# Performance work log

Hardware: AMD Instinct MI355X
Metric: run time of the kernel (lower is better)

Reference implementation:

```python
import jax, jax.numpy as jnp
import numpy as np

B, N, K = 4, 50000, 128   # batch, surface points, deformation nodes
GD = 128                  # SDF grid resolution (D=H=W)


def setup_inputs() -> dict:
    key = jax.random.key(0)
    ks = jax.random.split(key, 7)
    constants = jax.random.normal(ks[0], (B, K), dtype=jnp.float32)
    scales = 0.05 + 0.25 * jax.random.uniform(ks[1], (B, K), dtype=jnp.float32)
    # proper-ish rotations via QR of random matrices
    M = jax.random.normal(ks[2], (B, K, 3, 3), dtype=jnp.float32)
    rotations, _ = jnp.linalg.qr(M)
    centers = jax.random.uniform(ks[3], (B, K, 3), dtype=jnp.float32, minval=-0.5, maxval=0.5)
    surface_samples = jax.random.uniform(ks[4], (B, N, 6), dtype=jnp.float32, minval=-0.5, maxval=0.5)
    grid = jax.random.normal(ks[5], (B, GD, GD, GD), dtype=jnp.float32)
    # world2grid maps world [-0.5,0.5] -> grid index [0, GD-1]
    w2g = np.zeros((B, 4, 4), dtype=np.float32)
    w2g[:, 0, 0] = w2g[:, 1, 1] = w2g[:, 2, 2] = float(GD - 1)
    w2g[:, :3, 3] = float(GD - 1) / 2.0
    w2g[:, 3, 3] = 1.0
    world2grid = jnp.asarray(w2g)
    return {"constants": constants, "scales": scales, "rotations": rotations,
            "centers": centers, "surface_samples": surface_samples,
            "grid": grid, "world2grid": world2grid}


def _trilinear_border(vol, xyz):
    """torch grid_sample (5D, bilinear, align_corners=True, border) for one batch.
    vol: (D,H,W); xyz: (N,3) normalized coords in [-1,1], order (x,y,z)."""
    D, H, W = vol.shape
    x = jnp.clip((xyz[:, 0] + 1.0) * 0.5 * (W - 1), 0.0, W - 1)
    y = jnp.clip((xyz[:, 1] + 1.0) * 0.5 * (H - 1), 0.0, H - 1)
    z = jnp.clip((xyz[:, 2] + 1.0) * 0.5 * (D - 1), 0.0, D - 1)
    x0 = jnp.floor(x); y0 = jnp.floor(y); z0 = jnp.floor(z)
    fx = x - x0; fy = y - y0; fz = z - z0
    x0i = x0.astype(jnp.int32); x1i = jnp.minimum(x0i + 1, W - 1)
    y0i = y0.astype(jnp.int32); y1i = jnp.minimum(y0i + 1, H - 1)
    z0i = z0.astype(jnp.int32); z1i = jnp.minimum(z0i + 1, D - 1)
    c000 = vol[z0i, y0i, x0i]; c001 = vol[z0i, y0i, x1i]
    c010 = vol[z0i, y1i, x0i]; c011 = vol[z0i, y1i, x1i]
    c100 = vol[z1i, y0i, x0i]; c101 = vol[z1i, y0i, x1i]
    c110 = vol[z1i, y1i, x0i]; c111 = vol[z1i, y1i, x1i]
    c00 = c000 * (1 - fx) + c001 * fx
    c01 = c010 * (1 - fx) + c011 * fx
    c10 = c100 * (1 - fx) + c101 * fx
    c11 = c110 * (1 - fx) + c111 * fx
    c0 = c00 * (1 - fy) + c01 * fy
    c1 = c10 * (1 - fy) + c11 * fy
    return c0 * (1 - fz) + c1 * fz


def reference(constants, scales, rotations, centers, surface_samples, grid, world2grid):
    pts = surface_samples[..., :3]                       # (B,N,3)
    diff = pts[:, :, None, :] - centers[:, None, :, :]   # (B,N,K,3)  == p - t_source
    d2 = jnp.sum(diff * diff, axis=-1)                   # (B,N,K)
    # sample_rbf_weights with use_constants=True
    w = jnp.exp(-d2 / (2.0 * scales * scales)[:, None, :]) * (constants * constants)[:, None, :]
    w = w / jnp.sum(w, axis=-1, keepdims=True)           # normalize over nodes

    # target = roll batch by -1 (source_idx+1 mod B)
    R_t = jnp.roll(rotations, -1, axis=0)
    R_rel = jnp.einsum('bkij,bklj->bkil', R_t, rotations)       # R_target @ R_source^T
    c_t = jnp.roll(centers, -1, axis=0)
    transformed = jnp.einsum('bkij,bnkj->bnki', R_rel, diff) + c_t[:, None, :, :]
    blended = jnp.einsum('bnk,bnki->bni', w, transformed)        # (B,N,3)

    w2g_t = jnp.roll(world2grid, -1, axis=0)
    A = w2g_t[:, :3, :3]
    t = w2g_t[:, :3, 3]
    gcs = jnp.einsum('bij,bnj->bni', A, blended) + t[:, None, :]  # grid coords (x,y,z)

    D, H, W = grid.shape[1], grid.shape[2], grid.shape[3]
    denom = jnp.array([W - 1, H - 1, D - 1], dtype=gcs.dtype)
    gcs = 2.0 * (gcs / denom) - 1.0                               # normalize to [-1,1]

    grid_t = jnp.roll(grid, -1, axis=0)
    sdf = jax.vmap(_trilinear_border)(grid_t, gcs)                # (B,N)
    return jnp.sum(jnp.mean(sdf * sdf, axis=1))
```

## Files before the change

### kernel.cpp

```cpp
#include <hip/hip_runtime.h>
#include <stdint.h>

#define K_   128
#define GD_  128
#define PSTR 20
#define KPW  32

static __device__ __forceinline__ float fast_exp2(float x) {
#if __has_builtin(__builtin_amdgcn_exp2f)
    return __builtin_amdgcn_exp2f(x);
#else
    return exp2f(x);
#endif
}

__global__ void surf_param_kernel(
    const float* __restrict__ constants,
    const float* __restrict__ scales,
    const float* __restrict__ rotations,
    const float* __restrict__ centers,
    const float* __restrict__ w2g,
    float* __restrict__ params,
    float* __restrict__ out,
    int B)
{
    int idx = blockIdx.x * blockDim.x + threadIdx.x;
    if (idx == 0) out[0] = 0.0f;
    if (idx >= B * K_) return;
    int b = idx / K_, k = idx - b * K_;
    int bn = (b + 1 == B) ? 0 : (b + 1);
    const float L2E = 1.4426950408889634f;

    const float* R  = rotations + (size_t)(b  * K_ + k) * 9;
    const float* Rt = rotations + (size_t)(bn * K_ + k) * 9;
    float m[9];
#pragma unroll
    for (int i = 0; i < 3; ++i)
#pragma unroll
        for (int l = 0; l < 3; ++l)
            m[i * 3 + l] = Rt[i * 3 + 0] * R[l * 3 + 0]
                         + Rt[i * 3 + 1] * R[l * 3 + 1]
                         + Rt[i * 3 + 2] * R[l * 3 + 2];

    const float* Aw = w2g + (size_t)bn * 16;
    float G[9], A[9] = {Aw[0], Aw[1], Aw[2], Aw[4], Aw[5], Aw[6], Aw[8], Aw[9], Aw[10]};
    float T[3] = {Aw[3], Aw[7], Aw[11]};
#pragma unroll
    for (int i = 0; i < 3; ++i)
#pragma unroll
        for (int l = 0; l < 3; ++l)
            G[i * 3 + l] = A[i * 3 + 0] * m[0 * 3 + l]
                         + A[i * 3 + 1] * m[1 * 3 + l]
                         + A[i * 3 + 2] * m[2 * 3 + l];

    const float* c  = centers + (size_t)(b  * K_ + k) * 3;
    const float* ct = centers + (size_t)(bn * K_ + k) * 3;
    float c0 = c[0], c1 = c[1], c2 = c[2];
    float vw0 = ct[0] - (m[0] * c0 + m[1] * c1 + m[2] * c2);
    float vw1 = ct[1] - (m[3] * c0 + m[4] * c1 + m[5] * c2);
    float vw2 = ct[2] - (m[6] * c0 + m[7] * c1 + m[8] * c2);
    float v0 = A[0] * vw0 + A[1] * vw1 + A[2] * vw2 + T[0];
    float v1 = A[3] * vw0 + A[4] * vw1 + A[5] * vw2 + T[1];
    float v2 = A[6] * vw0 + A[7] * vw1 + A[8] * vw2 + T[2];

    float sig = scales[b * K_ + k];
    float s   = 1.0f / (2.0f * sig * sig);
    float con = constants[b * K_ + k];
    float s2n = -s * L2E;
    float r   = log2f(con * con) + s2n * (c0 * c0 + c1 * c1 + c2 * c2);

    float* o = params + (size_t)idx * PSTR;
    o[0] = G[0]; o[1] = G[1]; o[2] = G[2]; o[3] = G[3];
    o[4] = G[4]; o[5] = G[5]; o[6] = G[6]; o[7] = G[7];
    o[8] = G[8]; o[9] = v0;  o[10] = v1;  o[11] = v2;
    o[12] = -2.0f * s2n * c0;
    o[13] = -2.0f * s2n * c1;
    o[14] = -2.0f * s2n * c2;
    o[15] = r;
    o[16] = s2n;
    o[17] = 0.f; o[18] = 0.f; o[19] = 0.f;
}

__global__ __launch_bounds__(256) void surf_loss_kernel(
    const float* __restrict__ sp,
    const float* __restrict__ grid,
    const float* __restrict__ params,
    float* __restrict__ out,
    int N, int B, int bpb)
{
    __shared__ float  lds_par[K_ * PSTR];
    __shared__ float4 lds_part[4 * 4 * 64];
    __shared__ float  red[4];

    const int tid  = threadIdx.x;
    const int lane = tid & 63;
    const int wave = tid >> 6;
    const int blk  = blockIdx.x;
    const int b    = blk / bpb;
    const int base = (blk - b * bpb) * 256;
    const int bn   = (b + 1 == B) ? 0 : (b + 1);

    {
        const float4* Pv = (const float4*)(params + (size_t)b * K_ * PSTR);
        float4* Lv = (float4*)lds_par;
        for (int t = tid; t < K_ * PSTR / 4; t += 256)
            Lv[t] = Pv[t];
    }

    float px[4], py[4], pz[4], pq[4];
    float ax[4], ay[4], az[4], aw[4];
    const float* spb = sp + (size_t)b * N * 6;
#pragma unroll
    for (int j = 0; j < 4; ++j) {
        int n = base + j * 64 + lane;
        int nn = (n < N) ? n : 0;
        const float* q = spb + (size_t)nn * 6;
        px[j] = q[0]; py[j] = q[1]; pz[j] = q[2];
        pq[j] = px[j] * px[j] + py[j] * py[j] + pz[j] * pz[j];
        ax[j] = 0.f; ay[j] = 0.f; az[j] = 0.f; aw[j] = 0.f;
    }

    __syncthreads();

    const int k0 = wave * KPW;
#pragma unroll 2
    for (int kk = 0; kk < KPW; ++kk) {
        const float4* f = (const float4*)(lds_par + (k0 + kk) * PSTR);
        const float4 f0 = f[0];
        const float4 f1 = f[1];
        const float4 f2 = f[2];
        const float4 f3 = f[3];
        const float  s2 = lds_par[(k0 + kk) * PSTR + 16];
#pragma unroll
        for (int j = 0; j < 4; ++j) {
            float e = f3.w + f3.x * px[j] + f3.y * py[j] + f3.z * pz[j] + s2 * pq[j];
            float w = fast_exp2(e);
            float tx = f2.y + f0.x * px[j] + f0.y * py[j] + f0.z * pz[j];
            float ty = f2.z + f0.w * px[j] + f1.x * py[j] + f1.y * pz[j];
            float tz = f2.w + f1.z * px[j] + f1.w * py[j] + f2.x * pz[j];
            ax[j] += w * tx;
            ay[j] += w * ty;
            az[j] += w * tz;
            aw[j] += w;
        }
    }

#pragma unroll
    for (int j = 0; j < 4; ++j)
        lds_part[((wave * 4 + j) << 6) + lane] = make_float4(ax[j], ay[j], az[j], aw[j]);
    __syncthreads();

    float accum = 0.0f;
    {
        int n = base + wave * 64 + lane;
        if (n < N) {
            float sx = 0.f, sy = 0.f, sz = 0.f, sw = 0.f;
#pragma unroll
            for (int w = 0; w < 4; ++w) {
                float4 t = lds_part[((w * 4 + wave) << 6) + lane];
                sx += t.x; sy += t.y; sz += t.z; sw += t.w;
            }
            float inv = 1.0f / sw;
            float x = fminf(fmaxf(sx * inv, 0.0f), (float)(GD_ - 1));
            float y = fminf(fmaxf(sy * inv, 0.0f), (float)(GD_ - 1));
            float z = fminf(fmaxf(sz * inv, 0.0f), (float)(GD_ - 1));
            float x0f = floorf(x), y0f = floorf(y), z0f = floorf(z);
            float fx = x - x0f, fy = y - y0f, fz = z - z0f;
            int x0 = (int)x0f, y0 = (int)y0f, z0 = (int)z0f;
            int x1 = x0 + 1 > GD_ - 1 ? GD_ - 1 : x0 + 1;
            int y1 = y0 + 1 > GD_ - 1 ? GD_ - 1 : y0 + 1;
            int z1 = z0 + 1 > GD_ - 1 ? GD_ - 1 : z0 + 1;
            const float* gb = grid + (size_t)bn * GD_ * GD_ * GD_;
            int zy00 = (z0 * GD_ + y0) * GD_;
            int zy01 = (z0 * GD_ + y1) * GD_;
            int zy10 = (z1 * GD_ + y0) * GD_;
            int zy11 = (z1 * GD_ + y1) * GD_;
            float c000 = gb[zy00 + x0], c001 = gb[zy00 + x1];
            float c010 = gb[zy01 + x0], c011 = gb[zy01 + x1];
            float c100 = gb[zy10 + x0], c101 = gb[zy10 + x1];
            float c110 = gb[zy11 + x0], c111 = gb[zy11 + x1];
            float ofx = 1.0f - fx, ofy = 1.0f - fy, ofz = 1.0f - fz;
            float c00 = c000 * ofx + c001 * fx;
            float c01 = c010 * ofx + c011 * fx;
            float c10 = c100 * ofx + c101 * fx;
            float c11 = c110 * ofx + c111 * fx;
            float c0 = c00 * ofy + c01 * fy;
            float c1 = c10 * ofy + c11 * fy;
            float sdf = c0 * ofz + c1 * fz;
            accum = sdf * sdf;
        }
    }

#pragma unroll
    for (int off = 32; off > 0; off >>= 1)
        accum += __shfl_down(accum, off, 64);
    if (lane == 0) red[wave] = accum;
    __syncthreads();
    if (tid == 0)
        atomicAdd(out, (red[0] + red[1] + red[2] + red[3]) * (1.0f / (float)N));
}

extern "C" void kernel_launch(void* const* d_in, const int* in_sizes, int n_in,
                              void* d_out, int out_size, void* d_ws, size_t ws_size,
                              hipStream_t stream) {
    const float* constants = (const float*)d_in[0];
    const float* scales    = (const float*)d_in[1];
    const float* rotations = (const float*)d_in[2];
    const float* centers   = (const float*)d_in[3];
    const float* sp        = (const float*)d_in[4];
    const float* grid      = (const float*)d_in[5];
    const float* w2g       = (const float*)d_in[6];
    float* out = (float*)d_out;
    float* params = (float*)d_ws;

    const int B = in_sizes[6] / 16;
    const int N = in_sizes[4] / (6 * B);

    int np = B * K_;
    hipLaunchKernelGGL(surf_param_kernel, dim3((np + 255) / 256), dim3(256), 0, stream,
                       constants, scales, rotations, centers, w2g, params, out, B);

    const int bpb = (N + 255) / 256;
    hipLaunchKernelGGL(surf_loss_kernel, dim3(B * bpb), dim3(256), 0, stream,
                       sp, grid, params, out, N, B, bpb);
}
```

Baseline: 111.9 us.

## Broadcast node params via readlane and halve points per block

Each wave now loads its 32 nodes' parameters (packed as 10 float2 across 64 lanes) into registers once. Inside the node loop it broadcasts them with readlane instead of issuing LDS float4 reads every iteration. Points per block drop from 256 to 128, giving twice as many blocks and halving per-thread accumulators, and launch bounds request more waves per SIMD. The trade-off is more scalar readlane instructions and only half the waves doing the trilinear gather stage.

```diff
diff --git a/kernel.cpp b/kernel.cpp
--- a/kernel.cpp
+++ b/kernel.cpp
@@ -5,12 +5,21 @@
 #define GD_  128
 #define PSTR 20
 #define KPW  32
+#define PPB  128
 
 static __device__ __forceinline__ float fast_exp2(float x) {
 #if __has_builtin(__builtin_amdgcn_exp2f)
     return __builtin_amdgcn_exp2f(x);
 #else
     return exp2f(x);
+#endif
+}
+
+static __device__ __forceinline__ float bcast_lane(float v, int l) {
+#if __has_builtin(__builtin_amdgcn_readlane)
+    return __uint_as_float((unsigned)__builtin_amdgcn_readlane((int)__float_as_uint(v), l));
+#else
+    return __shfl(v, l, 64);
 #endif
 }
 
@@ -81,7 +90,7 @@
     o[17] = 0.f; o[18] = 0.f; o[19] = 0.f;
 }
 
-__global__ __launch_bounds__(256) void surf_loss_kernel(
+__global__ __launch_bounds__(256, 6) void surf_loss_kernel(
     const float* __restrict__ sp,
     const float* __restrict__ grid,
     const float* __restrict__ params,
@@ -89,7 +98,7 @@
     int N, int B, int bpb)
 {
     __shared__ float  lds_par[K_ * PSTR];
-    __shared__ float4 lds_part[4 * 4 * 64];
+    __shared__ float4 lds_part[4 * 2 * 64];
     __shared__ float  red[4];
 
     const int tid  = threadIdx.x;
@@ -97,7 +106,7 @@
     const int wave = tid >> 6;
     const int blk  = blockIdx.x;
     const int b    = blk / bpb;
-    const int base = (blk - b * bpb) * 256;
+    const int base = (blk - b * bpb) * PPB;
     const int bn   = (b + 1 == B) ? 0 : (b + 1);
 
     {
@@ -107,11 +116,11 @@
             Lv[t] = Pv[t];
     }
 
-    float px[4], py[4], pz[4], pq[4];
-    float ax[4], ay[4], az[4], aw[4];
+    float px[2], py[2], pz[2], pq[2];
+    float ax[2], ay[2], az[2], aw[2];
     const float* spb = sp + (size_t)b * N * 6;
 #pragma unroll
-    for (int j = 0; j < 4; ++j) {
+    for (int j = 0; j < 2; ++j) {
         int n = base + j * 64 + lane;
         int nn = (n < N) ? n : 0;
         const float* q = spb + (size_t)nn * 6;
@@ -123,21 +132,31 @@
     __syncthreads();
 
     const int k0 = wave * KPW;
+    float c0, c1, c2, c3, c4, c5, c6, c7, c8, c9;
+    {
+        const float2* f2p = (const float2*)(lds_par + k0 * PSTR) + (size_t)lane * 5;
+        float2 d0 = f2p[0], d1 = f2p[1], d2 = f2p[2], d3 = f2p[3], d4 = f2p[4];
+        c0 = d0.x; c1 = d0.y; c2 = d1.x; c3 = d1.y; c4 = d2.x;
+        c5 = d2.y; c6 = d3.x; c7 = d3.y; c8 = d4.x; c9 = d4.y;
+    }
+
 #pragma unroll 2
     for (int kk = 0; kk < KPW; ++kk) {
-        const float4* f = (const float4*)(lds_par + (k0 + kk) * PSTR);
-        const float4 f0 = f[0];
-        const float4 f1 = f[1];
-        const float4 f2 = f[2];
-        const float4 f3 = f[3];
-        const float  s2 = lds_par[(k0 + kk) * PSTR + 16];
-#pragma unroll
-        for (int j = 0; j < 4; ++j) {
-            float e = f3.w + f3.x * px[j] + f3.y * py[j] + f3.z * pz[j] + s2 * pq[j];
+        const int l0 = kk + kk, l1 = l0 + 1;
+        const float g0 = bcast_lane(c0, l0), g1 = bcast_lane(c1, l0), g2 = bcast_lane(c2, l0);
+        const float g3 = bcast_lane(c3, l0), g4 = bcast_lane(c4, l0), g5 = bcast_lane(c5, l0);
+        const float g6 = bcast_lane(c6, l0), g7 = bcast_lane(c7, l0), g8 = bcast_lane(c8, l0);
+        const float v0 = bcast_lane(c9, l0);
+        const float v1 = bcast_lane(c0, l1), v2 = bcast_lane(c1, l1);
+        const float q0 = bcast_lane(c2, l1), q1 = bcast_lane(c3, l1), q2 = bcast_lane(c4, l1);
+        const float rr = bcast_lane(c5, l1), s2 = bcast_lane(c6, l1);
+#pragma unroll
+        for (int j = 0; j < 2; ++j) {
+            float e = rr + q0 * px[j] + q1 * py[j] + q2 * pz[j] + s2 * pq[j];
             float w = fast_exp2(e);
-            float tx = f2.y + f0.x * px[j] + f0.y * py[j] + f0.z * pz[j];
-            float ty = f2.z + f0.w * px[j] + f1.x * py[j] + f1.y * pz[j];
-            float tz = f2.w + f1.z * px[j] + f1.w * py[j] + f2.x * pz[j];
+            float tx = v0 + g0 * px[j] + g1 * py[j] + g2 * pz[j];
+            float ty = v1 + g3 * px[j] + g4 * py[j] + g5 * pz[j];
+            float tz = v2 + g6 * px[j] + g7 * py[j] + g8 * pz[j];
             ax[j] += w * tx;
             ay[j] += w * ty;
             az[j] += w * tz;
@@ -146,18 +165,18 @@
     }
 
 #pragma unroll
-    for (int j = 0; j < 4; ++j)
-        lds_part[((wave * 4 + j) << 6) + lane] = make_float4(ax[j], ay[j], az[j], aw[j]);
+    for (int j = 0; j < 2; ++j)
+        lds_part[((wave * 2 + j) << 6) + lane] = make_float4(ax[j], ay[j], az[j], aw[j]);
     __syncthreads();
 
     float accum = 0.0f;
-    {
+    if (wave < 2) {
         int n = base + wave * 64 + lane;
         if (n < N) {
             float sx = 0.f, sy = 0.f, sz = 0.f, sw = 0.f;
 #pragma unroll
             for (int w = 0; w < 4; ++w) {
-                float4 t = lds_part[((w * 4 + wave) << 6) + lane];
+                float4 t = lds_part[((w * 2 + wave) << 6) + lane];
                 sx += t.x; sy += t.y; sz += t.z; sw += t.w;
             }
             float inv = 1.0f / sw;
@@ -184,9 +203,9 @@
             float c01 = c010 * ofx + c011 * fx;
             float c10 = c100 * ofx + c101 * fx;
             float c11 = c110 * ofx + c111 * fx;
-            float c0 = c00 * ofy + c01 * fy;
-            float c1 = c10 * ofy + c11 * fy;
-            float sdf = c0 * ofz + c1 * fz;
+            float cc0 = c00 * ofy + c01 * fy;
+            float cc1 = c10 * ofy + c11 * fy;
+            float sdf = cc0 * ofz + cc1 * fz;
             accum = sdf * sdf;
         }
     }
@@ -220,7 +239,7 @@
     hipLaunchKernelGGL(surf_param_kernel, dim3((np + 255) / 256), dim3(256), 0, stream,
                        constants, scales, rotations, centers, w2g, params, out, B);
 
-    const int bpb = (N + 255) / 256;
+    const int bpb = (N + PPB - 1) / PPB;
     hipLaunchKernelGGL(surf_loss_kernel, dim3(B * bpb), dim3(256), 0, stream,
                        sp, grid, params, out, N, B, bpb);
 }
```

Result: slower. 121.6 us (+8.7%).
